# Performance work log

Measured on AMD Instinct MI355X. Metric: run time of the kernel, lower is better.

## Reference

```python
import jax, jax.numpy as jnp
from jax import lax
import numpy as np

I_SIZE = 1024
H_SIZE = 1024
BATCH = 64
SEQ = 512


def _xavier(key, shape):
    # matches nn.init.xavier_uniform_ for 2D params
    fan_in, fan_out = shape
    limit = float(np.sqrt(6.0 / (fan_in + fan_out)))
    return jax.random.uniform(key, shape, jnp.float32, -limit, limit)


def setup_inputs() -> dict:
    key = jax.random.key(0)
    ks = jax.random.split(key, 9)
    x = jax.random.normal(ks[0], (BATCH, SEQ, I_SIZE), jnp.float32)
    w_ii = _xavier(ks[1], (I_SIZE, H_SIZE))
    w_hi = _xavier(ks[2], (H_SIZE, H_SIZE))
    w_if = _xavier(ks[3], (I_SIZE, H_SIZE))
    w_hf = _xavier(ks[4], (H_SIZE, H_SIZE))
    w_ig = _xavier(ks[5], (I_SIZE, H_SIZE))
    w_hg = _xavier(ks[6], (H_SIZE, H_SIZE))
    w_io = _xavier(ks[7], (I_SIZE, H_SIZE))
    w_ho = _xavier(ks[8], (H_SIZE, H_SIZE))
    zb = jnp.zeros((H_SIZE,), jnp.float32)  # init_hidden zeros all 1D params
    return {
        "x": x,
        "w_ii": w_ii, "b_ii": zb, "w_hi": w_hi, "b_hi": zb,
        "w_if": w_if, "b_if": zb, "w_hf": w_hf, "b_hf": zb,
        "w_ig": w_ig, "b_ig": zb, "w_hg": w_hg, "b_hg": zb,
        "w_io": w_io, "b_io": zb, "w_ho": w_ho, "b_ho": zb,
    }


def reference(x, w_ii, b_ii, w_hi, b_hi, w_if, b_if, w_hf, b_hf,
              w_ig, b_ig, w_hg, b_hg, w_io, b_io, w_ho, b_ho):
    # Fuse the 4 input-side and 4 hidden-side GEMMs into one each (same math).
    Wi = jnp.concatenate([w_ii, w_if, w_ig, w_io], axis=1)        # (I, 4H)
    Wh = jnp.concatenate([w_hi, w_hf, w_hg, w_ho], axis=1)        # (H, 4H)
    b = jnp.concatenate([b_ii + b_hi, b_if + b_hf, b_ig + b_hg, b_io + b_ho])  # (4H,)
    # Precompute all input projections in one big GEMM: (B, S, 4H)
    x_proj = jnp.einsum('bsi,ih->bsh', x, Wi) + b

    B = x.shape[0]
    H = w_hi.shape[0]
    h0 = jnp.zeros((B, H), x.dtype)

    def step(carry, xt):
        h, c = carry
        gates = xt + h @ Wh                       # (B, 4H)
        i, f, g, o = jnp.split(gates, 4, axis=-1)
        i = jax.nn.sigmoid(i)
        f = jax.nn.sigmoid(f)
        g = jnp.tanh(g)
        o = jax.nn.sigmoid(o)
        c = c * f + i * g
        h = o * jnp.tanh(c)
        return (h, c), None

    (h_t, c_t), _ = lax.scan(step, (h0, h0), jnp.swapaxes(x_proj, 0, 1))
    return (h_t, c_t)
```

## Files before the change

kernel.cpp:

```cpp
#include <hip/hip_runtime.h>


typedef __bf16 bf16x8 __attribute__((ext_vector_type(8)));
typedef float f32x4 __attribute__((ext_vector_type(4)));
typedef unsigned int uint4v __attribute__((ext_vector_type(4)));

__device__ __forceinline__ unsigned short f2bf(float f) {
    unsigned int u = __float_as_uint(f);
    u = (u + 0x7FFFu + ((u >> 16) & 1u)) >> 16;
    return (unsigned short)u;
}
__device__ __forceinline__ float bf2f(unsigned short u) {
    return __uint_as_float((unsigned int)u << 16);
}

__global__ __launch_bounds__(256) void pack_wT(
    const float* __restrict__ w0, const float* __restrict__ w1,
    const float* __restrict__ w2, const float* __restrict__ w3,
    const float* __restrict__ w4, const float* __restrict__ w5,
    const float* __restrict__ w6, const float* __restrict__ w7,
    unsigned short* __restrict__ wiT, unsigned short* __restrict__ whT)
{
    __shared__ float tl[64][65];
    int bid = blockIdx.x;
    int mi = bid >> 8;
    int tile = bid & 255;
    int tk = tile >> 4, tj = tile & 15;
    const float* w;
    int gate = mi & 3;
    if (mi < 4) w = (gate == 0) ? w0 : (gate == 1) ? w1 : (gate == 2) ? w2 : w3;
    else        w = (gate == 0) ? w4 : (gate == 1) ? w5 : (gate == 2) ? w6 : w7;
    unsigned short* out = (mi < 4) ? wiT : whT;
    int tx = threadIdx.x & 63, ty = threadIdx.x >> 6;
    #pragma unroll
    for (int i = 0; i < 16; i++) {
        int k = i * 4 + ty;
        tl[k][tx] = w[(long)(tk * 64 + k) * 1024 + tj * 64 + tx];
    }
    __syncthreads();
    #pragma unroll
    for (int i = 0; i < 16; i++) {
        int j = i * 4 + ty;
        out[(long)(gate * 1024 + tj * 64 + j) * 1024 + tk * 64 + tx] = f2bf(tl[tx][j]);
    }
}

__global__ __launch_bounds__(256) void pack_misc(
    const float* __restrict__ bi0, const float* __restrict__ bh0,
    const float* __restrict__ bi1, const float* __restrict__ bh1,
    const float* __restrict__ bi2, const float* __restrict__ bh2,
    const float* __restrict__ bi3, const float* __restrict__ bh3,
    float* __restrict__ bias, unsigned int* __restrict__ hbuf_u,
    unsigned int* __restrict__ flags)
{
    int idx = blockIdx.x * 256 + threadIdx.x;
    hbuf_u[idx] = 0u;
    if (idx < 4096) {
        int g = idx >> 10, j = idx & 1023;
        const float* bi = (g == 0) ? bi0 : (g == 1) ? bi1 : (g == 2) ? bi2 : bi3;
        const float* bh = (g == 0) ? bh0 : (g == 1) ? bh1 : (g == 2) ? bh2 : bh3;
        bias[idx] = bi[j] + bh[j];
    }
    if (idx < 256) flags[idx] = 0u;
}

__global__ __launch_bounds__(256, 2) void gemm_xproj(
    const float* __restrict__ x, const unsigned short* __restrict__ wiT,
    unsigned short* __restrict__ xp)
{
    __shared__ unsigned short sA[128 * 72];
    __shared__ unsigned short sB[128 * 72];
    int bid = blockIdx.x;
    int mt = bid >> 5, nt = bid & 31;
    long m0 = (long)mt * 128;
    int n0 = nt * 128;
    int tid = threadIdx.x;
    int lane = tid & 63, wv = tid >> 6;
    int quad = lane >> 4, l15 = lane & 15;
    int wm = wv & 1, wn = wv >> 1;

    f32x4 acc[4][4];
    #pragma unroll
    for (int a = 0; a < 4; a++)
        #pragma unroll
        for (int b = 0; b < 4; b++)
            acc[a][b] = (f32x4){0.f, 0.f, 0.f, 0.f};

    for (int kb = 0; kb < 16; kb++) {
        int k0 = kb * 64;
        #pragma unroll
        for (int i = 0; i < 8; i++) {
            int ch = tid + i * 256;
            int row = ch >> 4, q = ch & 15;
            float4 v = *(const float4*)&x[(m0 + row) * 1024 + k0 + q * 4];
            uint2 p;
            p.x = (unsigned int)f2bf(v.x) | ((unsigned int)f2bf(v.y) << 16);
            p.y = (unsigned int)f2bf(v.z) | ((unsigned int)f2bf(v.w) << 16);
            *(uint2*)&sA[row * 72 + q * 4] = p;
        }
        #pragma unroll
        for (int i = 0; i < 4; i++) {
            int ch = tid + i * 256;
            int row = ch >> 3, q = ch & 7;
            uint4 v = *(const uint4*)&wiT[(long)(n0 + row) * 1024 + k0 + q * 8];
            *(uint4*)&sB[row * 72 + q * 8] = v;
        }
        __syncthreads();
        #pragma unroll
        for (int ks = 0; ks < 2; ks++) {
            bf16x8 af[4], bfr[4];
            #pragma unroll
            for (int mi2 = 0; mi2 < 4; mi2++)
                af[mi2] = *(const bf16x8*)&sA[(wm * 64 + mi2 * 16 + l15) * 72 + ks * 32 + quad * 8];
            #pragma unroll
            for (int ni = 0; ni < 4; ni++)
                bfr[ni] = *(const bf16x8*)&sB[(wn * 64 + ni * 16 + l15) * 72 + ks * 32 + quad * 8];
            #pragma unroll
            for (int mi2 = 0; mi2 < 4; mi2++)
                #pragma unroll
                for (int ni = 0; ni < 4; ni++)
                    acc[mi2][ni] = __builtin_amdgcn_mfma_f32_16x16x32_bf16(
                        af[mi2], bfr[ni], acc[mi2][ni], 0, 0, 0);
        }
        __syncthreads();
    }
    #pragma unroll
    for (int mi2 = 0; mi2 < 4; mi2++)
        #pragma unroll
        for (int ni = 0; ni < 4; ni++)
            #pragma unroll
            for (int r = 0; r < 4; r++) {
                long row = m0 + wm * 64 + mi2 * 16 + quad * 4 + r;
                int col = n0 + wn * 64 + ni * 16 + l15;
                int h = col & 1023, gate = col >> 10;
                xp[row * 4096 + h * 4 + gate] = f2bf(acc[mi2][ni][r]);
            }
}

__global__ __launch_bounds__(256, 2) void lstm_scan(
    const unsigned short* __restrict__ xp, const unsigned short* __restrict__ whT,
    const float* __restrict__ bias, unsigned short* __restrict__ hbuf,
    unsigned int* __restrict__ flags, float* __restrict__ out)
{
    __shared__ unsigned short hl[16 * 1032];
    __shared__ float xch[4][16][16];

    int bid = blockIdx.x;
    int g = bid >> 6, s = bid & 63;
    int tid = threadIdx.x;
    int lane = tid & 63, wv = tid >> 6;
    int quad = lane >> 4, l15 = lane & 15;

    bf16x8 bfrag[32];
    {
        const unsigned short* bp = whT + (long)(wv * 1024 + s * 16 + l15) * 1024 + quad * 8;
        #pragma unroll
        for (int kk = 0; kk < 32; kk++)
            bfrag[kk] = *(const bf16x8*)(bp + kk * 32);
    }

    int row = tid >> 4, col = tid & 15;
    float b4[4];
    #pragma unroll
    for (int gg = 0; gg < 4; gg++) b4[gg] = bias[gg * 1024 + s * 16 + col];

    float c = 0.f;
    const unsigned int* myflags = flags + g * 64 + lane;
    unsigned int* myflag = flags + g * 64 + s;
    const char* hb0 = (const char*)(hbuf + g * 16 * 1024);
    const char* hb1 = (const char*)(hbuf + 4 * 16 * 1024 + g * 16 * 1024);
    unsigned short* hw0 = hbuf + g * 16 * 1024;
    unsigned short* hw1 = hbuf + 4 * 16 * 1024 + g * 16 * 1024;

    for (int t = 0; t < 512; t++) {
        const unsigned short* xr = xp + ((long)(g * 16 + row) * 512 + t) * 4096
                                      + (s * 16 + col) * 4;
        uint2 xg = *(const uint2*)xr;
        float xpi = bf2f((unsigned short)(xg.x & 0xFFFF));
        float xpf = bf2f((unsigned short)(xg.x >> 16));
        float xpg = bf2f((unsigned short)(xg.y & 0xFFFF));
        float xpo = bf2f((unsigned short)(xg.y >> 16));

        if (t > 0) {
            while (true) {
                unsigned int f = __hip_atomic_load(myflags, __ATOMIC_RELAXED,
                                                   __HIP_MEMORY_SCOPE_AGENT);
                if (__all((int)(f >= (unsigned int)t))) break;
                __builtin_amdgcn_s_sleep(1);
            }
        }

        const char* hsrc = (t & 1) ? hb1 : hb0;
        uint4v hv[8];
        #pragma unroll
        for (int i = 0; i < 8; i++) {
            int ch = tid + i * 256;
            int r2 = ch >> 7, off = ch & 127;
            const void* p = hsrc + r2 * 2048 + off * 16;
            asm volatile("global_load_dwordx4 %0, %1, off sc0 sc1"
                         : "=v"(hv[i]) : "v"(p) : "memory");
        }
        asm volatile("s_waitcnt vmcnt(0)" ::: "memory");
        #pragma unroll
        for (int i = 0; i < 8; i++) {
            int ch = tid + i * 256;
            int r2 = ch >> 7, off = ch & 127;
            *(uint4v*)&hl[r2 * 1032 + off * 8] = hv[i];
        }
        __syncthreads();

        f32x4 acc = {0.f, 0.f, 0.f, 0.f};
        #pragma unroll
        for (int kk = 0; kk < 32; kk++) {
            bf16x8 af = *(const bf16x8*)&hl[l15 * 1032 + kk * 32 + quad * 8];
            acc = __builtin_amdgcn_mfma_f32_16x16x32_bf16(af, bfrag[kk], acc, 0, 0, 0);
        }
        #pragma unroll
        for (int r = 0; r < 4; r++)
            xch[wv][quad * 4 + r][l15] = acc[r];
        __syncthreads();

        float gi = xch[0][row][col] + xpi + b4[0];
        float gf = xch[1][row][col] + xpf + b4[1];
        float gg_ = xch[2][row][col] + xpg + b4[2];
        float go = xch[3][row][col] + xpo + b4[3];
        float iv = 1.f / (1.f + __expf(-gi));
        float fv = 1.f / (1.f + __expf(-gf));
        float gv = 1.f - 2.f / (__expf(2.f * gg_) + 1.f);
        float ov = 1.f / (1.f + __expf(-go));
        c = c * fv + iv * gv;
        float h = ov * (1.f - 2.f / (__expf(2.f * c) + 1.f));

        if (t == 511) {
            out[(g * 16 + row) * 1024 + s * 16 + col] = h;
            out[65536 + (g * 16 + row) * 1024 + s * 16 + col] = c;
        } else {
            unsigned short* hdst = (t & 1) ? hw0 : hw1;
            __hip_atomic_store(&hdst[row * 1024 + s * 16 + col], f2bf(h),
                               __ATOMIC_RELAXED, __HIP_MEMORY_SCOPE_AGENT);
            __syncthreads();
            if (tid == 0)
                __hip_atomic_store(myflag, (unsigned int)(t + 1),
                                   __ATOMIC_RELAXED, __HIP_MEMORY_SCOPE_AGENT);
        }
    }
}

extern "C" void kernel_launch(void* const* d_in, const int* in_sizes, int n_in,
                              void* d_out, int out_size, void* d_ws, size_t ws_size,
                              hipStream_t stream)
{
    const float* x    = (const float*)d_in[0];
    const float* w_ii = (const float*)d_in[1];
    const float* b_ii = (const float*)d_in[2];
    const float* w_hi = (const float*)d_in[3];
    const float* b_hi = (const float*)d_in[4];
    const float* w_if = (const float*)d_in[5];
    const float* b_if = (const float*)d_in[6];
    const float* w_hf = (const float*)d_in[7];
    const float* b_hf = (const float*)d_in[8];
    const float* w_ig = (const float*)d_in[9];
    const float* b_ig = (const float*)d_in[10];
    const float* w_hg = (const float*)d_in[11];
    const float* b_hg = (const float*)d_in[12];
    const float* w_io = (const float*)d_in[13];
    const float* b_io = (const float*)d_in[14];
    const float* w_ho = (const float*)d_in[15];
    const float* b_ho = (const float*)d_in[16];

    const size_t OFF_XPJ  = 0;
    const size_t OFF_WIT  = 268435456;
    const size_t OFF_WHT  = 276824064;
    const size_t OFF_BIAS = 285212672;
    const size_t OFF_HBUF = 285229056;
    const size_t OFF_FLG  = 285491200;
    const size_t NEEDED   = 285493248;
    if (ws_size < NEEDED) return;

    char* ws = (char*)d_ws;
    unsigned short* xpj      = (unsigned short*)(ws + OFF_XPJ);
    unsigned short* wiT      = (unsigned short*)(ws + OFF_WIT);
    unsigned short* whT      = (unsigned short*)(ws + OFF_WHT);
    float*          bias     = (float*)(ws + OFF_BIAS);
    unsigned short* hbuf     = (unsigned short*)(ws + OFF_HBUF);
    unsigned int*   flags    = (unsigned int*)(ws + OFF_FLG);

    pack_wT<<<2048, 256, 0, stream>>>(w_ii, w_if, w_ig, w_io,
                                      w_hi, w_hf, w_hg, w_ho, wiT, whT);
    pack_misc<<<256, 256, 0, stream>>>(b_ii, b_hi, b_if, b_hf, b_ig, b_hg, b_io, b_ho,
                                       bias, (unsigned int*)hbuf, flags);
    gemm_xproj<<<8192, 256, 0, stream>>>(x, wiT, xpj);
    lstm_scan<<<256, 256, 0, stream>>>(xpj, whT, bias, hbuf, flags, (float*)d_out);
}
```

Baseline: 2.377 ms.

## Tag hidden state with step counter, drop flags; bf16 pre-pass and LDS DMA in GEMM

The recurrent scan no longer uses per-block flags and a second barrier. Each hidden value is stored as a 32-bit word holding a bf16 value and a 16-bit step tag, and readers spin until every tag matches the expected step. This removes a flag round trip and a barrier from the serial critical path, but doubles the hidden-buffer traffic. Separately, x is converted to bf16 in its own kernel, and the projection GEMM loads tiles straight into an XOR-swizzled LDS layout through global_load_lds, at the cost of an extra pass over x.

```diff
diff --git a/kernel.cpp b/kernel.cpp
--- a/kernel.cpp
+++ b/kernel.cpp
@@ -50,8 +50,7 @@
     const float* __restrict__ bi1, const float* __restrict__ bh1,
     const float* __restrict__ bi2, const float* __restrict__ bh2,
     const float* __restrict__ bi3, const float* __restrict__ bh3,
-    float* __restrict__ bias, unsigned int* __restrict__ hbuf_u,
-    unsigned int* __restrict__ flags)
+    float* __restrict__ bias, unsigned int* __restrict__ hbuf_u)
 {
     int idx = blockIdx.x * 256 + threadIdx.x;
     hbuf_u[idx] = 0u;
@@ -61,15 +60,28 @@
         const float* bh = (g == 0) ? bh0 : (g == 1) ? bh1 : (g == 2) ? bh2 : bh3;
         bias[idx] = bi[j] + bh[j];
     }
-    if (idx < 256) flags[idx] = 0u;
+}
+
+__global__ __launch_bounds__(256) void x2bf(const float* __restrict__ x,
+                                            unsigned short* __restrict__ xbf)
+{
+    long i = ((long)blockIdx.x * 256 + threadIdx.x) * 8;
+    float4 a = *(const float4*)&x[i];
+    float4 b = *(const float4*)&x[i + 4];
+    uint4 v;
+    v.x = (unsigned int)f2bf(a.x) | ((unsigned int)f2bf(a.y) << 16);
+    v.y = (unsigned int)f2bf(a.z) | ((unsigned int)f2bf(a.w) << 16);
+    v.z = (unsigned int)f2bf(b.x) | ((unsigned int)f2bf(b.y) << 16);
+    v.w = (unsigned int)f2bf(b.z) | ((unsigned int)f2bf(b.w) << 16);
+    *(uint4*)&xbf[i] = v;
 }
 
 __global__ __launch_bounds__(256, 2) void gemm_xproj(
-    const float* __restrict__ x, const unsigned short* __restrict__ wiT,
+    const unsigned short* __restrict__ xbf, const unsigned short* __restrict__ wiT,
     unsigned short* __restrict__ xp)
 {
-    __shared__ unsigned short sA[128 * 72];
-    __shared__ unsigned short sB[128 * 72];
+    __shared__ unsigned short sA[128 * 64];
+    __shared__ unsigned short sB[128 * 64];
     int bid = blockIdx.x;
     int mt = bid >> 5, nt = bid & 31;
     long m0 = (long)mt * 128;
@@ -89,32 +101,35 @@
     for (int kb = 0; kb < 16; kb++) {
         int k0 = kb * 64;
         #pragma unroll
-        for (int i = 0; i < 8; i++) {
-            int ch = tid + i * 256;
-            int row = ch >> 4, q = ch & 15;
-            float4 v = *(const float4*)&x[(m0 + row) * 1024 + k0 + q * 4];
-            uint2 p;
-            p.x = (unsigned int)f2bf(v.x) | ((unsigned int)f2bf(v.y) << 16);
-            p.y = (unsigned int)f2bf(v.z) | ((unsigned int)f2bf(v.w) << 16);
-            *(uint2*)&sA[row * 72 + q * 4] = p;
-        }
-        #pragma unroll
-        for (int i = 0; i < 4; i++) {
-            int ch = tid + i * 256;
-            int row = ch >> 3, q = ch & 7;
-            uint4 v = *(const uint4*)&wiT[(long)(n0 + row) * 1024 + k0 + q * 8];
-            *(uint4*)&sB[row * 72 + q * 8] = v;
+        for (int j = 0; j < 4; j++) {
+            int Lb = wv * 256 + j * 64;
+            int row = (Lb >> 3) + (lane >> 3);
+            int csrc = (lane & 7) ^ ((lane >> 3) & 7);
+            const unsigned short* gA = xbf + (m0 + row) * 1024 + k0 + csrc * 8;
+            __builtin_amdgcn_global_load_lds(
+                (const __attribute__((address_space(1))) unsigned int*)gA,
+                (__attribute__((address_space(3))) unsigned int*)&sA[Lb * 8],
+                16, 0, 0);
+            const unsigned short* gB = wiT + (long)(n0 + row) * 1024 + k0 + csrc * 8;
+            __builtin_amdgcn_global_load_lds(
+                (const __attribute__((address_space(1))) unsigned int*)gB,
+                (__attribute__((address_space(3))) unsigned int*)&sB[Lb * 8],
+                16, 0, 0);
         }
         __syncthreads();
         #pragma unroll
         for (int ks = 0; ks < 2; ks++) {
             bf16x8 af[4], bfr[4];
             #pragma unroll
-            for (int mi2 = 0; mi2 < 4; mi2++)
-                af[mi2] = *(const bf16x8*)&sA[(wm * 64 + mi2 * 16 + l15) * 72 + ks * 32 + quad * 8];
-            #pragma unroll
-            for (int ni = 0; ni < 4; ni++)
-                bfr[ni] = *(const bf16x8*)&sB[(wn * 64 + ni * 16 + l15) * 72 + ks * 32 + quad * 8];
+            for (int mi2 = 0; mi2 < 4; mi2++) {
+                int r = wm * 64 + mi2 * 16 + l15;
+                af[mi2] = *(const bf16x8*)&sA[r * 64 + ((ks * 4 + quad) ^ (r & 7)) * 8];
+            }
+            #pragma unroll
+            for (int ni = 0; ni < 4; ni++) {
+                int r = wn * 64 + ni * 16 + l15;
+                bfr[ni] = *(const bf16x8*)&sB[r * 64 + ((ks * 4 + quad) ^ (r & 7)) * 8];
+            }
             #pragma unroll
             for (int mi2 = 0; mi2 < 4; mi2++)
                 #pragma unroll
@@ -137,10 +152,10 @@
             }
 }
 
-__global__ __launch_bounds__(256, 2) void lstm_scan(
+__global__ __launch_bounds__(256, 1) void lstm_scan(
     const unsigned short* __restrict__ xp, const unsigned short* __restrict__ whT,
-    const float* __restrict__ bias, unsigned short* __restrict__ hbuf,
-    unsigned int* __restrict__ flags, float* __restrict__ out)
+    const float* __restrict__ bias, unsigned int* __restrict__ hbuf,
+    float* __restrict__ out)
 {
     __shared__ unsigned short hl[16 * 1032];
     __shared__ float xch[4][16][16];
@@ -165,61 +180,73 @@
     for (int gg = 0; gg < 4; gg++) b4[gg] = bias[gg * 1024 + s * 16 + col];
 
     float c = 0.f;
-    const unsigned int* myflags = flags + g * 64 + lane;
-    unsigned int* myflag = flags + g * 64 + s;
-    const char* hb0 = (const char*)(hbuf + g * 16 * 1024);
-    const char* hb1 = (const char*)(hbuf + 4 * 16 * 1024 + g * 16 * 1024);
-    unsigned short* hw0 = hbuf + g * 16 * 1024;
-    unsigned short* hw1 = hbuf + 4 * 16 * 1024 + g * 16 * 1024;
+    unsigned int* hbu0 = hbuf + g * 16 * 1024;
+    unsigned int* hbu1 = hbuf + 4 * 16 * 1024 + g * 16 * 1024;
 
     for (int t = 0; t < 512; t++) {
         const unsigned short* xr = xp + ((long)(g * 16 + row) * 512 + t) * 4096
                                       + (s * 16 + col) * 4;
         uint2 xg = *(const uint2*)xr;
+
+        unsigned int expect = (unsigned int)t & 0xFFFFu;
+        const unsigned int* hsrc = (t & 1) ? hbu1 : hbu0;
+
+        {
+            const unsigned int* sp = hsrc + (tid >> 6) * 1024 + (tid & 63) * 16;
+            while (true) {
+                unsigned int w;
+                asm volatile("global_load_dword %0, %1, off sc0 sc1\n\ts_waitcnt vmcnt(0)"
+                             : "=v"(w) : "v"(sp) : "memory");
+                if (__all((int)((w & 0xFFFFu) == expect))) break;
+                __builtin_amdgcn_s_sleep(1);
+            }
+        }
+
+        uint4v hv[16];
+        unsigned int pend = 0xFFFFu;
+        while (pend) {
+            #pragma unroll
+            for (int i = 0; i < 16; i++)
+                if (pend & (1u << i)) {
+                    const void* p = (const char*)hsrc + (tid + i * 256) * 16;
+                    asm volatile("global_load_dwordx4 %0, %1, off sc0 sc1"
+                                 : "=v"(hv[i]) : "v"(p) : "memory");
+                }
+            asm volatile("s_waitcnt vmcnt(0)" ::: "memory");
+            #pragma unroll
+            for (int i = 0; i < 16; i++)
+                if (pend & (1u << i)) {
+                    if (((hv[i].x & 0xFFFFu) == expect) && ((hv[i].y & 0xFFFFu) == expect) &&
+                        ((hv[i].z & 0xFFFFu) == expect) && ((hv[i].w & 0xFFFFu) == expect))
+                        pend &= ~(1u << i);
+                }
+        }
+        #pragma unroll
+        for (int i = 0; i < 16; i++) {
+            int ch = tid + i * 256;
+            int r2 = ch >> 8, off = ch & 255;
+            uint2 pk;
+            pk.x = (hv[i].x >> 16) | (hv[i].y & 0xFFFF0000u);
+            pk.y = (hv[i].z >> 16) | (hv[i].w & 0xFFFF0000u);
+            *(uint2*)&hl[r2 * 1032 + off * 4] = pk;
+        }
+        __syncthreads();
+
+        f32x4 acc = {0.f, 0.f, 0.f, 0.f};
+        #pragma unroll
+        for (int kk = 0; kk < 32; kk++) {
+            bf16x8 af = *(const bf16x8*)&hl[l15 * 1032 + kk * 32 + quad * 8];
+            acc = __builtin_amdgcn_mfma_f32_16x16x32_bf16(af, bfrag[kk], acc, 0, 0, 0);
+        }
+        #pragma unroll
+        for (int r = 0; r < 4; r++)
+            xch[wv][quad * 4 + r][l15] = acc[r];
+        __syncthreads();
+
         float xpi = bf2f((unsigned short)(xg.x & 0xFFFF));
         float xpf = bf2f((unsigned short)(xg.x >> 16));
         float xpg = bf2f((unsigned short)(xg.y & 0xFFFF));
         float xpo = bf2f((unsigned short)(xg.y >> 16));
-
-        if (t > 0) {
-            while (true) {
-                unsigned int f = __hip_atomic_load(myflags, __ATOMIC_RELAXED,
-                                                   __HIP_MEMORY_SCOPE_AGENT);
-                if (__all((int)(f >= (unsigned int)t))) break;
-                __builtin_amdgcn_s_sleep(1);
-            }
-        }
-
-        const char* hsrc = (t & 1) ? hb1 : hb0;
-        uint4v hv[8];
-        #pragma unroll
-        for (int i = 0; i < 8; i++) {
-            int ch = tid + i * 256;
-            int r2 = ch >> 7, off = ch & 127;
-            const void* p = hsrc + r2 * 2048 + off * 16;
-            asm volatile("global_load_dwordx4 %0, %1, off sc0 sc1"
-                         : "=v"(hv[i]) : "v"(p) : "memory");
-        }
-        asm volatile("s_waitcnt vmcnt(0)" ::: "memory");
-        #pragma unroll
-        for (int i = 0; i < 8; i++) {
-            int ch = tid + i * 256;
-            int r2 = ch >> 7, off = ch & 127;
-            *(uint4v*)&hl[r2 * 1032 + off * 8] = hv[i];
-        }
-        __syncthreads();
-
-        f32x4 acc = {0.f, 0.f, 0.f, 0.f};
-        #pragma unroll
-        for (int kk = 0; kk < 32; kk++) {
-            bf16x8 af = *(const bf16x8*)&hl[l15 * 1032 + kk * 32 + quad * 8];
-            acc = __builtin_amdgcn_mfma_f32_16x16x32_bf16(af, bfrag[kk], acc, 0, 0, 0);
-        }
-        #pragma unroll
-        for (int r = 0; r < 4; r++)
-            xch[wv][quad * 4 + r][l15] = acc[r];
-        __syncthreads();
-
         float gi = xch[0][row][col] + xpi + b4[0];
         float gf = xch[1][row][col] + xpf + b4[1];
         float gg_ = xch[2][row][col] + xpg + b4[2];
@@ -235,13 +262,10 @@
             out[(g * 16 + row) * 1024 + s * 16 + col] = h;
             out[65536 + (g * 16 + row) * 1024 + s * 16 + col] = c;
         } else {
-            unsigned short* hdst = (t & 1) ? hw0 : hw1;
-            __hip_atomic_store(&hdst[row * 1024 + s * 16 + col], f2bf(h),
-                               __ATOMIC_RELAXED, __HIP_MEMORY_SCOPE_AGENT);
-            __syncthreads();
-            if (tid == 0)
-                __hip_atomic_store(myflag, (unsigned int)(t + 1),
-                                   __ATOMIC_RELAXED, __HIP_MEMORY_SCOPE_AGENT);
+            unsigned int word = ((unsigned int)f2bf(h) << 16)
+                              | ((unsigned int)(t + 1) & 0xFFFFu);
+            unsigned int* hdst = ((t & 1) ? hbu0 : hbu1) + row * 1024 + s * 16 + col;
+            __hip_atomic_store(hdst, word, __ATOMIC_RELAXED, __HIP_MEMORY_SCOPE_AGENT);
         }
     }
 }
@@ -269,26 +293,27 @@
     const float* b_ho = (const float*)d_in[16];
 
     const size_t OFF_XPJ  = 0;
-    const size_t OFF_WIT  = 268435456;
-    const size_t OFF_WHT  = 276824064;
-    const size_t OFF_BIAS = 285212672;
-    const size_t OFF_HBUF = 285229056;
-    const size_t OFF_FLG  = 285491200;
-    const size_t NEEDED   = 285493248;
+    const size_t OFF_XBF  = 268435456;
+    const size_t OFF_WIT  = 335544320;
+    const size_t OFF_WHT  = 343932928;
+    const size_t OFF_BIAS = 352321536;
+    const size_t OFF_HBUF = 352337920;
+    const size_t NEEDED   = 352862208;
     if (ws_size < NEEDED) return;
 
     char* ws = (char*)d_ws;
-    unsigned short* xpj      = (unsigned short*)(ws + OFF_XPJ);
-    unsigned short* wiT      = (unsigned short*)(ws + OFF_WIT);
-    unsigned short* whT      = (unsigned short*)(ws + OFF_WHT);
-    float*          bias     = (float*)(ws + OFF_BIAS);
-    unsigned short* hbuf     = (unsigned short*)(ws + OFF_HBUF);
-    unsigned int*   flags    = (unsigned int*)(ws + OFF_FLG);
+    unsigned short* xpj  = (unsigned short*)(ws + OFF_XPJ);
+    unsigned short* xbf  = (unsigned short*)(ws + OFF_XBF);
+    unsigned short* wiT  = (unsigned short*)(ws + OFF_WIT);
+    unsigned short* whT  = (unsigned short*)(ws + OFF_WHT);
+    float*          bias = (float*)(ws + OFF_BIAS);
+    unsigned int*   hbuf = (unsigned int*)(ws + OFF_HBUF);
 
     pack_wT<<<2048, 256, 0, stream>>>(w_ii, w_if, w_ig, w_io,
                                       w_hi, w_hf, w_hg, w_ho, wiT, whT);
-    pack_misc<<<256, 256, 0, stream>>>(b_ii, b_hi, b_if, b_hf, b_ig, b_hg, b_io, b_ho,
-                                       bias, (unsigned int*)hbuf, flags);
-    gemm_xproj<<<8192, 256, 0, stream>>>(x, wiT, xpj);
-    lstm_scan<<<256, 256, 0, stream>>>(xpj, whT, bias, hbuf, flags, (float*)d_out);
-}
+    pack_misc<<<512, 256, 0, stream>>>(b_ii, b_hi, b_if, b_hf, b_ig, b_hg, b_io, b_ho,
+                                       bias, hbuf);
+    x2bf<<<16384, 256, 0, stream>>>(x, xbf);
+    gemm_xproj<<<8192, 256, 0, stream>>>(xbf, wiT, xpj);
+    lstm_scan<<<256, 256, 0, stream>>>(xpj, whT, bias, hbuf, (float*)d_out);
+}
```

Measured after the change: 2.731 ms. +14.9%, slower.
